# Kernel tuning notes

Hardware: AMD Instinct MI355X
Metric: run time of the kernel (lower is better)

The kernel has to match this reference:

```python
import jax, jax.numpy as jnp
import numpy as np

BN_EPS = 1e-5


def setup_inputs() -> dict:
    key = jax.random.key(0)
    k1, k2, k3, k4, k5 = jax.random.split(key, 5)
    N, E, D = 100000, 1600000, 128
    x = jax.random.normal(k1, (N, D), dtype=jnp.float32)
    edge_index = jax.random.randint(k2, (2, E), 0, N, dtype=jnp.int64)
    # GCNConv linear weight (PyG stores as [out, in], applied as x @ W.T) + post-agg bias
    W = jax.random.normal(k3, (D, D), dtype=jnp.float32) * (1.0 / np.sqrt(D))
    b = jax.random.normal(k4, (D,), dtype=jnp.float32) * 0.01
    gamma = jnp.ones((D,), dtype=jnp.float32)
    beta = jnp.zeros((D,), dtype=jnp.float32)
    return {"x": x, "edge_index": edge_index, "W": W, "b": b, "gamma": gamma, "beta": beta}


def reference(x, edge_index, W, b, gamma, beta):
    N = x.shape[0]
    src, dst = edge_index[0], edge_index[1]
    # GCN symmetric normalization (no self loops): deg over dst with unit weights
    deg = jax.ops.segment_sum(jnp.ones(src.shape[0], dtype=x.dtype), dst, num_segments=N)
    dinv = jnp.where(deg > 0, jax.lax.rsqrt(jnp.maximum(deg, 1.0)), 0.0)
    norm = dinv[src] * dinv[dst]                      # [E]
    xw = x @ W.T                                      # [N, D] linear transform first (fewer FLOPs)
    msg = xw[src] * norm[:, None]                     # [E, D] gather + scale
    agg = jax.ops.segment_sum(msg, dst, num_segments=N) + b  # [N, D] scatter-add + bias
    # BatchNorm1d over nodes (training-mode batch stats, biased variance)
    mu = jnp.mean(agg, axis=0)
    var = jnp.mean(jnp.square(agg - mu), axis=0)
    h = (agg - mu) * jax.lax.rsqrt(var + BN_EPS) * gamma + beta
    h = jax.nn.relu(h)
    return h + x
```

## Files before the change

kernel.cpp:

```cpp
#include <hip/hip_runtime.h>

#define DD 128
#define BN_EPS 1e-5f
#define BINSHIFT 8
#define EPB 8192
#define CAP 6144

typedef __attribute__((ext_vector_type(8))) short bf16x8;
typedef __attribute__((ext_vector_type(4))) float f32x4;

static __device__ __forceinline__ size_t rowoff(int r) { return (size_t)r * DD; }

static __device__ __forceinline__ ushort f2bf(float f) {
  unsigned u = __float_as_uint(f);
  unsigned r = (u + 0x7fffu + ((u >> 16) & 1u)) >> 16;
  return (ushort)r;
}

__global__ __launch_bounds__(256) void k_convW(const float* __restrict__ W,
                                               ushort* __restrict__ Wb) {
  int t = threadIdx.x;
#pragma unroll
  for (int i = 0; i < 16; ++i) {
    int f = i * 256 + t;
    int row = f >> 5, c4 = f & 31;
    float4 w = reinterpret_cast<const float4*>(W)[f];
    ushort4 p = make_ushort4(f2bf(w.x), f2bf(w.y), f2bf(w.z), f2bf(w.w));
    int chunk = (c4 >> 1) ^ (row & 7);
    *reinterpret_cast<ushort4*>(reinterpret_cast<char*>(Wb) + row * 256 +
                                chunk * 16 + (c4 & 1) * 8) = p;
  }
}

__global__ __launch_bounds__(256) void k_binscatter(const int* __restrict__ src,
                                                    const int* __restrict__ dst,
                                                    int* __restrict__ gcursor,
                                                    unsigned* __restrict__ stg,
                                                    int E, int NB) {
  __shared__ int hist[1024];
  __shared__ int base[1024];
  int t = threadIdx.x;
  long long e0 = (long long)blockIdx.x * EPB;
  int eend = (int)((e0 + EPB < E) ? e0 + EPB : E);
  for (int i = t; i < NB; i += 256) hist[i] = 0;
  __syncthreads();
  for (int i = (int)e0 + t; i < eend; i += 256) atomicAdd(&hist[dst[i] >> BINSHIFT], 1);
  __syncthreads();
  for (int i = t; i < NB; i += 256) {
    int c = hist[i];
    base[i] = c ? (i * CAP + atomicAdd(&gcursor[i], c)) : 0;
    hist[i] = 0;
  }
  __syncthreads();
  for (int i = (int)e0 + t; i < eend; i += 256) {
    int d = dst[i];
    int bin = d >> BINSHIFT;
    unsigned v = ((unsigned)(d & 255) << 24) | (unsigned)src[i];
    int p = atomicAdd(&hist[bin], 1);
    stg[base[bin] + p] = v;
  }
}

__global__ __launch_bounds__(256) void k_binsort(const unsigned* __restrict__ stg,
                                                 const int* __restrict__ gcursor,
                                                 int* __restrict__ ssrc,
                                                 int* __restrict__ offs,
                                                 int* __restrict__ oend,
                                                 float* __restrict__ dinv,
                                                 int N) {
  __shared__ int hist[256];
  __shared__ int scanb[256];
  int b = blockIdx.x;
  int t = threadIdx.x;
  int beg = b * CAP;
  int end = beg + gcursor[b];
  int nloc = N - b * 256;
  if (nloc > 256) nloc = 256;
  hist[t] = 0;
  __syncthreads();
  for (int i = beg + t; i < end; i += 256) atomicAdd(&hist[stg[i] >> 24], 1);
  __syncthreads();
  int h = hist[t];
  scanb[t] = h;
  __syncthreads();
  for (int off = 1; off < 256; off <<= 1) {
    int u = (t >= off) ? scanb[t - off] : 0;
    __syncthreads();
    scanb[t] += u;
    __syncthreads();
  }
  int myexcl = scanb[t] - h;
  __syncthreads();
  scanb[t] = myexcl;
  hist[t] = 0;
  int node = b * 256 + t;
  if (t < nloc) {
    offs[node] = beg + myexcl;
    oend[node] = beg + myexcl + h;
    dinv[node] = h > 0 ? rsqrtf((float)h) : 0.f;
  }
  __syncthreads();
  for (int i = beg + t; i < end; i += 256) {
    unsigned v = stg[i];
    int loc = v >> 24;
    int p = atomicAdd(&hist[loc], 1);
    ssrc[beg + scanb[loc] + p] = (int)(v & 0xFFFFFFu);
  }
}

__global__ __launch_bounds__(256) void k_gemm_mfma(const float* __restrict__ x,
                                                   const ushort* __restrict__ Wb,
                                                   const float* __restrict__ dinv,
                                                   ushort* __restrict__ xwb, int N) {
  __shared__ ushort Abuf[128 * 128];
  __shared__ ushort Bbuf[128 * 128];
  int t = threadIdx.x;
  int brow = blockIdx.x * 128;
  int wid = t >> 6, lane = t & 63;

  {
    const char* gW = reinterpret_cast<const char*>(Wb);
    char* lB = reinterpret_cast<char*>(Bbuf);
#pragma unroll
    for (int i = 0; i < 8; ++i) {
      int off = i * 4096 + wid * 1024;
      __builtin_amdgcn_global_load_lds(
          (const __attribute__((address_space(1))) void*)(gW + off + lane * 16),
          (__attribute__((address_space(3))) void*)(lB + off), 16, 0, 0);
    }
  }
  for (int i = 0; i < 16; ++i) {
    int f = i * 256 + t;
    int row = f >> 5, c4 = f & 31;
    int grow = brow + row;
    float4 v = make_float4(0.f, 0.f, 0.f, 0.f);
    if (grow < N) v = reinterpret_cast<const float4*>(x)[(size_t)grow * 32 + c4];
    ushort4 p = make_ushort4(f2bf(v.x), f2bf(v.y), f2bf(v.z), f2bf(v.w));
    int chunk = (c4 >> 1) ^ (row & 7);
    *reinterpret_cast<ushort4*>(reinterpret_cast<char*>(Abuf) + row * 256 +
                                chunk * 16 + (c4 & 1) * 8) = p;
  }
  __syncthreads();

  int kgrp = lane >> 4;
  int r0 = wid * 32 + (lane & 15);
  int r1 = r0 + 16;
  f32x4 acc[2][8];
#pragma unroll
  for (int rt = 0; rt < 2; ++rt)
#pragma unroll
    for (int cf = 0; cf < 8; ++cf) acc[rt][cf] = (f32x4){0.f, 0.f, 0.f, 0.f};

  const char* Ab = reinterpret_cast<const char*>(Abuf);
  const char* Bb = reinterpret_cast<const char*>(Bbuf);
#pragma unroll
  for (int ks = 0; ks < 4; ++ks) {
    int c = ks * 4 + kgrp;
    bf16x8 a0 = *reinterpret_cast<const bf16x8*>(Ab + r0 * 256 + ((c ^ (r0 & 7)) * 16));
    bf16x8 a1 = *reinterpret_cast<const bf16x8*>(Ab + r1 * 256 + ((c ^ (r1 & 7)) * 16));
#pragma unroll
    for (int cf = 0; cf < 8; ++cf) {
      int bc = cf * 16 + (lane & 15);
      bf16x8 bv = *reinterpret_cast<const bf16x8*>(Bb + bc * 256 + ((c ^ (bc & 7)) * 16));
      acc[0][cf] = __builtin_amdgcn_mfma_f32_16x16x32_bf16(a0, bv, acc[0][cf], 0, 0, 0);
      acc[1][cf] = __builtin_amdgcn_mfma_f32_16x16x32_bf16(a1, bv, acc[1][cf], 0, 0, 0);
    }
  }

#pragma unroll
  for (int rt = 0; rt < 2; ++rt) {
#pragma unroll
    for (int j = 0; j < 4; ++j) {
      int gr = brow + wid * 32 + rt * 16 + (lane >> 4) * 4 + j;
      if (gr < N) {
        float sc = dinv[gr];
        ushort* orow = xwb + (size_t)gr * DD + (lane & 15);
#pragma unroll
        for (int cf = 0; cf < 8; ++cf) orow[cf * 16] = f2bf(acc[rt][cf][j] * sc);
      }
    }
  }
}

__global__ __launch_bounds__(256) void k_aggregate(const int* __restrict__ offs,
                                                   const int* __restrict__ oend,
                                                   const int* __restrict__ ssrc,
                                                   const float* __restrict__ dinv,
                                                   const float* __restrict__ bvec,
                                                   const ushort* __restrict__ xwb,
                                                   float* __restrict__ agg,
                                                   float* __restrict__ stats, int N) {
  __shared__ float red[1024];
  int t = threadIdx.x;
  int wid = t >> 6, lane = t & 63;
  float bc0 = bvec[2 * lane], bc1 = bvec[2 * lane + 1];
  float s0 = 0.f, q0 = 0.f, s1 = 0.f, q1 = 0.f;
  const unsigned laneb = lane * 2;

  for (int d = blockIdx.x * 4 + wid; d < N; d += gridDim.x * 4) {
    int off = offs[d], end = oend[d];
    float a0 = 0.f, a1 = 0.f, b0 = 0.f, b1 = 0.f;
    float c0 = 0.f, c1 = 0.f, e0 = 0.f, e1 = 0.f;
    int j = off;
    for (; j + 8 <= end; j += 8) {
      int sA = ssrc[j],     sB = ssrc[j + 1], sC = ssrc[j + 2], sD = ssrc[j + 3];
      int sE = ssrc[j + 4], sF = ssrc[j + 5], sG = ssrc[j + 6], sH = ssrc[j + 7];
      unsigned v0 = *reinterpret_cast<const unsigned*>(xwb + (size_t)sA * DD + laneb);
      unsigned v1 = *reinterpret_cast<const unsigned*>(xwb + (size_t)sB * DD + laneb);
      unsigned v2 = *reinterpret_cast<const unsigned*>(xwb + (size_t)sC * DD + laneb);
      unsigned v3 = *reinterpret_cast<const unsigned*>(xwb + (size_t)sD * DD + laneb);
      unsigned v4 = *reinterpret_cast<const unsigned*>(xwb + (size_t)sE * DD + laneb);
      unsigned v5 = *reinterpret_cast<const unsigned*>(xwb + (size_t)sF * DD + laneb);
      unsigned v6 = *reinterpret_cast<const unsigned*>(xwb + (size_t)sG * DD + laneb);
      unsigned v7 = *reinterpret_cast<const unsigned*>(xwb + (size_t)sH * DD + laneb);
      a0 += __uint_as_float(v0 << 16);
      a1 += __uint_as_float(v0 & 0xffff0000u);
      b0 += __uint_as_float(v1 << 16);
      b1 += __uint_as_float(v1 & 0xffff0000u);
      c0 += __uint_as_float(v2 << 16);
      c1 += __uint_as_float(v2 & 0xffff0000u);
      e0 += __uint_as_float(v3 << 16);
      e1 += __uint_as_float(v3 & 0xffff0000u);
      a0 += __uint_as_float(v4 << 16);
      a1 += __uint_as_float(v4 & 0xffff0000u);
      b0 += __uint_as_float(v5 << 16);
      b1 += __uint_as_float(v5 & 0xffff0000u);
      c0 += __uint_as_float(v6 << 16);
      c1 += __uint_as_float(v6 & 0xffff0000u);
      e0 += __uint_as_float(v7 << 16);
      e1 += __uint_as_float(v7 & 0xffff0000u);
    }
    if (j + 4 <= end) {
      int sA = ssrc[j], sB = ssrc[j + 1], sC = ssrc[j + 2], sD = ssrc[j + 3];
      unsigned v0 = *reinterpret_cast<const unsigned*>(xwb + (size_t)sA * DD + laneb);
      unsigned v1 = *reinterpret_cast<const unsigned*>(xwb + (size_t)sB * DD + laneb);
      unsigned v2 = *reinterpret_cast<const unsigned*>(xwb + (size_t)sC * DD + laneb);
      unsigned v3 = *reinterpret_cast<const unsigned*>(xwb + (size_t)sD * DD + laneb);
      a0 += __uint_as_float(v0 << 16);
      a1 += __uint_as_float(v0 & 0xffff0000u);
      b0 += __uint_as_float(v1 << 16);
      b1 += __uint_as_float(v1 & 0xffff0000u);
      c0 += __uint_as_float(v2 << 16);
      c1 += __uint_as_float(v2 & 0xffff0000u);
      e0 += __uint_as_float(v3 << 16);
      e1 += __uint_as_float(v3 & 0xffff0000u);
      j += 4;
    }
    for (; j < end; ++j) {
      int sA = ssrc[j];
      unsigned v0 = *reinterpret_cast<const unsigned*>(xwb + (size_t)sA * DD + laneb);
      a0 += __uint_as_float(v0 << 16);
      a1 += __uint_as_float(v0 & 0xffff0000u);
    }
    float dd = dinv[d];
    float r0 = ((a0 + b0) + (c0 + e0)) * dd;
    float r1 = ((a1 + b1) + (c1 + e1)) * dd;
    reinterpret_cast<float2*>(agg + rowoff(d))[lane] = make_float2(r0, r1);
    float t0 = r0 + bc0, t1 = r1 + bc1;
    s0 += t0; q0 += t0 * t0;
    s1 += t1; q1 += t1 * t1;
  }

  float4* rw = reinterpret_cast<float4*>(red);
  rw[wid * 64 + lane] = make_float4(s0, q0, s1, q1);
  __syncthreads();
  {
    float v = red[t] + red[256 + t] + red[512 + t] + red[768 + t];
    int ln = t >> 2, k = t & 3;
    int col = 2 * ln + (k >> 1);
    int rep = blockIdx.x & 7;
    atomicAdd(&stats[rep * 256 + (k & 1) * 128 + col], v);
  }
}

__global__ __launch_bounds__(256) void k_final(float* __restrict__ agg,
                                               const float* __restrict__ x,
                                               const float* __restrict__ b,
                                               const float* __restrict__ gamma,
                                               const float* __restrict__ beta,
                                               const float* __restrict__ stats,
                                               float invN, int N) {
  __shared__ float muS[DD], rsS[DD];
  int t = threadIdx.x;
  if (t < DD) {
    float s = 0.f, q = 0.f;
#pragma unroll
    for (int rep = 0; rep < 8; ++rep) {
      s += stats[rep * 256 + t];
      q += stats[rep * 256 + 128 + t];
    }
    float mu = s * invN;
    float var = q * invN - mu * mu;
    muS[t] = mu;
    rsS[t] = rsqrtf(var + BN_EPS);
  }
  __syncthreads();

  long long i = (long long)blockIdx.x * 256 + threadIdx.x;
  long long stride = (long long)gridDim.x * 256;
  long long total = (long long)N * (DD / 4);
  const float4* __restrict__ x4 = reinterpret_cast<const float4*>(x);
  float4* __restrict__ a4 = reinterpret_cast<float4*>(agg);
  const float4* __restrict__ b4 = reinterpret_cast<const float4*>(b);
  const float4* __restrict__ g4 = reinterpret_cast<const float4*>(gamma);
  const float4* __restrict__ be4 = reinterpret_cast<const float4*>(beta);
  const float4* muL = reinterpret_cast<const float4*>(muS);
  const float4* rsL = reinterpret_cast<const float4*>(rsS);
  for (; i < total; i += stride) {
    int c4 = (int)(i & (DD / 4 - 1));
    float4 v = a4[i];
    float4 xv = x4[i];
    float4 bb = b4[c4], gg = g4[c4], be = be4[c4], mm = muL[c4], rr = rsL[c4];
    float4 o;
    o.x = fmaxf((v.x + bb.x - mm.x) * rr.x * gg.x + be.x, 0.f) + xv.x;
    o.y = fmaxf((v.y + bb.y - mm.y) * rr.y * gg.y + be.y, 0.f) + xv.y;
    o.z = fmaxf((v.z + bb.z - mm.z) * rr.z * gg.z + be.z, 0.f) + xv.z;
    o.w = fmaxf((v.w + bb.w - mm.w) * rr.w * gg.w + be.w, 0.f) + xv.w;
    a4[i] = o;
  }
}

extern "C" void kernel_launch(void* const* d_in, const int* in_sizes, int n_in,
                              void* d_out, int out_size, void* d_ws, size_t ws_size,
                              hipStream_t stream) {
  const float* x = (const float*)d_in[0];
  const int* ei = (const int*)d_in[1];
  const float* W = (const float*)d_in[2];
  const float* b = (const float*)d_in[3];
  const float* gamma = (const float*)d_in[4];
  const float* beta = (const float*)d_in[5];
  int N = in_sizes[0] / DD;
  int E = in_sizes[1] / 2;
  float* out = (float*)d_out;
  const int* src = ei;
  const int* dst = ei + E;
  int NB = (N + 255) >> BINSHIFT;

  ushort* xwb = (ushort*)d_ws;
  ushort* Wb = xwb + (size_t)N * DD;
  unsigned* stg = (unsigned*)(Wb + DD * DD);
  int* ssrc = (int*)(stg + (size_t)NB * CAP);
  int* offs = ssrc + (size_t)NB * CAP;
  int* oend = offs + N;
  float* dinv = (float*)(oend + N);
  int* gcursor = (int*)(dinv + N);
  float* stats = (float*)(gcursor + 1024);

  hipMemsetAsync(gcursor, 0, 1024 * sizeof(int) + 2048 * sizeof(float), stream);

  k_convW<<<1, 256, 0, stream>>>(W, Wb);

  int nchunk = (E + EPB - 1) / EPB;
  k_binscatter<<<nchunk, 256, 0, stream>>>(src, dst, gcursor, stg, E, NB);
  k_binsort<<<NB, 256, 0, stream>>>(stg, gcursor, ssrc, offs, oend, dinv, N);

  int gG = (N + 127) / 128;
  k_gemm_mfma<<<gG, 256, 0, stream>>>(x, Wb, dinv, xwb, N);

  k_aggregate<<<2048, 256, 0, stream>>>(offs, oend, ssrc, dinv, b, xwb, out, stats, N);

  k_final<<<2048, 256, 0, stream>>>(out, x, b, gamma, beta, stats, 1.0f / (float)N, N);
}
```

Measured before the change: 163.3 us.

## Merge W conversion into scatter, run binsort alongside GEMM, stage agg in bf16

The W bf16 conversion becomes an extra block of the edge scatter kernel. Binsort and the GEMM now share one launch, which removes the GEMM's dependence on dinv. The source-side dinv scaling moves into the aggregation loop as an extra gathered load per edge. Aggregated rows are written to a bf16 scratch buffer when workspace allows, halving the intermediate write and read traffic in the final kernel, at the cost of extra rounding error and more per-edge loads.

```diff
diff --git a/kernel.cpp b/kernel.cpp
--- a/kernel.cpp
+++ b/kernel.cpp
@@ -1,4 +1,5 @@
 #include <hip/hip_runtime.h>
+#include <hip/hip_bf16.h>
 
 #define DD 128
 #define BN_EPS 1e-5f
@@ -12,34 +13,35 @@
 static __device__ __forceinline__ size_t rowoff(int r) { return (size_t)r * DD; }
 
 static __device__ __forceinline__ ushort f2bf(float f) {
-  unsigned u = __float_as_uint(f);
-  unsigned r = (u + 0x7fffu + ((u >> 16) & 1u)) >> 16;
-  return (ushort)r;
-}
-
-__global__ __launch_bounds__(256) void k_convW(const float* __restrict__ W,
-                                               ushort* __restrict__ Wb) {
+  __hip_bfloat16 h = __float2bfloat16(f);
+  return __builtin_bit_cast(ushort, h);
+}
+static __device__ __forceinline__ float bf_lo(unsigned u) { return __uint_as_float(u << 16); }
+static __device__ __forceinline__ float bf_hi(unsigned u) { return __uint_as_float(u & 0xffff0000u); }
+
+__global__ __launch_bounds__(256) void k_scatter_convw(const int* __restrict__ src,
+                                                       const int* __restrict__ dst,
+                                                       int* __restrict__ gcursor,
+                                                       unsigned* __restrict__ stg,
+                                                       const float* __restrict__ W,
+                                                       ushort* __restrict__ Wb,
+                                                       int E, int NB, int nchunk) {
   int t = threadIdx.x;
-#pragma unroll
-  for (int i = 0; i < 16; ++i) {
-    int f = i * 256 + t;
-    int row = f >> 5, c4 = f & 31;
-    float4 w = reinterpret_cast<const float4*>(W)[f];
-    ushort4 p = make_ushort4(f2bf(w.x), f2bf(w.y), f2bf(w.z), f2bf(w.w));
-    int chunk = (c4 >> 1) ^ (row & 7);
-    *reinterpret_cast<ushort4*>(reinterpret_cast<char*>(Wb) + row * 256 +
-                                chunk * 16 + (c4 & 1) * 8) = p;
-  }
-}
-
-__global__ __launch_bounds__(256) void k_binscatter(const int* __restrict__ src,
-                                                    const int* __restrict__ dst,
-                                                    int* __restrict__ gcursor,
-                                                    unsigned* __restrict__ stg,
-                                                    int E, int NB) {
+  if (blockIdx.x == (unsigned)nchunk) {
+#pragma unroll
+    for (int i = 0; i < 16; ++i) {
+      int f = i * 256 + t;
+      int row = f >> 5, c4 = f & 31;
+      float4 w = reinterpret_cast<const float4*>(W)[f];
+      ushort4 p = make_ushort4(f2bf(w.x), f2bf(w.y), f2bf(w.z), f2bf(w.w));
+      int chunk = (c4 >> 1) ^ (row & 7);
+      *reinterpret_cast<ushort4*>(reinterpret_cast<char*>(Wb) + row * 256 +
+                                  chunk * 16 + (c4 & 1) * 8) = p;
+    }
+    return;
+  }
   __shared__ int hist[1024];
   __shared__ int base[1024];
-  int t = threadIdx.x;
   long long e0 = (long long)blockIdx.x * EPB;
   int eend = (int)((e0 + EPB < E) ? e0 + EPB : E);
   for (int i = t; i < NB; i += 256) hist[i] = 0;
@@ -61,66 +63,68 @@
   }
 }
 
-__global__ __launch_bounds__(256) void k_binsort(const unsigned* __restrict__ stg,
-                                                 const int* __restrict__ gcursor,
-                                                 int* __restrict__ ssrc,
-                                                 int* __restrict__ offs,
-                                                 int* __restrict__ oend,
-                                                 float* __restrict__ dinv,
-                                                 int N) {
-  __shared__ int hist[256];
-  __shared__ int scanb[256];
-  int b = blockIdx.x;
+__global__ __launch_bounds__(256) void k_gemm_binsort(const float* __restrict__ x,
+                                                      const ushort* __restrict__ Wb,
+                                                      ushort* __restrict__ xwb,
+                                                      const unsigned* __restrict__ stg,
+                                                      const int* __restrict__ gcursor,
+                                                      int* __restrict__ ssrc,
+                                                      int* __restrict__ offs,
+                                                      int* __restrict__ oend,
+                                                      float* __restrict__ dinv,
+                                                      int N, int gG) {
+  __shared__ char pool[65536];
   int t = threadIdx.x;
-  int beg = b * CAP;
-  int end = beg + gcursor[b];
-  int nloc = N - b * 256;
-  if (nloc > 256) nloc = 256;
-  hist[t] = 0;
-  __syncthreads();
-  for (int i = beg + t; i < end; i += 256) atomicAdd(&hist[stg[i] >> 24], 1);
-  __syncthreads();
-  int h = hist[t];
-  scanb[t] = h;
-  __syncthreads();
-  for (int off = 1; off < 256; off <<= 1) {
-    int u = (t >= off) ? scanb[t - off] : 0;
-    __syncthreads();
-    scanb[t] += u;
-    __syncthreads();
-  }
-  int myexcl = scanb[t] - h;
-  __syncthreads();
-  scanb[t] = myexcl;
-  hist[t] = 0;
-  int node = b * 256 + t;
-  if (t < nloc) {
-    offs[node] = beg + myexcl;
-    oend[node] = beg + myexcl + h;
-    dinv[node] = h > 0 ? rsqrtf((float)h) : 0.f;
-  }
-  __syncthreads();
-  for (int i = beg + t; i < end; i += 256) {
-    unsigned v = stg[i];
-    int loc = v >> 24;
-    int p = atomicAdd(&hist[loc], 1);
-    ssrc[beg + scanb[loc] + p] = (int)(v & 0xFFFFFFu);
-  }
-}
-
-__global__ __launch_bounds__(256) void k_gemm_mfma(const float* __restrict__ x,
-                                                   const ushort* __restrict__ Wb,
-                                                   const float* __restrict__ dinv,
-                                                   ushort* __restrict__ xwb, int N) {
-  __shared__ ushort Abuf[128 * 128];
-  __shared__ ushort Bbuf[128 * 128];
-  int t = threadIdx.x;
+
+  if ((int)blockIdx.x >= gG) {
+    int* hist = (int*)pool;
+    int* scanb = (int*)(pool + 1024);
+    int b = blockIdx.x - gG;
+    int beg = b * CAP;
+    int end = beg + gcursor[b];
+    int nloc = N - b * 256;
+    if (nloc > 256) nloc = 256;
+    hist[t] = 0;
+    __syncthreads();
+    for (int i = beg + t; i < end; i += 256) atomicAdd(&hist[stg[i] >> 24], 1);
+    __syncthreads();
+    int h = hist[t];
+    scanb[t] = h;
+    __syncthreads();
+    for (int off = 1; off < 256; off <<= 1) {
+      int u = (t >= off) ? scanb[t - off] : 0;
+      __syncthreads();
+      scanb[t] += u;
+      __syncthreads();
+    }
+    int myexcl = scanb[t] - h;
+    __syncthreads();
+    scanb[t] = myexcl;
+    hist[t] = 0;
+    int node = b * 256 + t;
+    if (t < nloc) {
+      offs[node] = beg + myexcl;
+      oend[node] = beg + myexcl + h;
+      dinv[node] = h > 0 ? rsqrtf((float)h) : 0.f;
+    }
+    __syncthreads();
+    for (int i = beg + t; i < end; i += 256) {
+      unsigned v = stg[i];
+      int loc = v >> 24;
+      int p = atomicAdd(&hist[loc], 1);
+      ssrc[beg + scanb[loc] + p] = (int)(v & 0xFFFFFFu);
+    }
+    return;
+  }
+
+  ushort* Abuf = (ushort*)pool;
+  ushort* Bbuf = (ushort*)(pool + 32768);
   int brow = blockIdx.x * 128;
   int wid = t >> 6, lane = t & 63;
 
   {
     const char* gW = reinterpret_cast<const char*>(Wb);
-    char* lB = reinterpret_cast<char*>(Bbuf);
+    char* lB = pool + 32768;
 #pragma unroll
     for (int i = 0; i < 8; ++i) {
       int off = i * 4096 + wid * 1024;
@@ -173,10 +177,9 @@
     for (int j = 0; j < 4; ++j) {
       int gr = brow + wid * 32 + rt * 16 + (lane >> 4) * 4 + j;
       if (gr < N) {
-        float sc = dinv[gr];
         ushort* orow = xwb + (size_t)gr * DD + (lane & 15);
 #pragma unroll
-        for (int cf = 0; cf < 8; ++cf) orow[cf * 16] = f2bf(acc[rt][cf][j] * sc);
+        for (int cf = 0; cf < 8; ++cf) orow[cf * 16] = f2bf(acc[rt][cf][j]);
       }
     }
   }
@@ -189,6 +192,7 @@
                                                    const float* __restrict__ bvec,
                                                    const ushort* __restrict__ xwb,
                                                    float* __restrict__ agg,
+                                                   ushort* __restrict__ aggb,
                                                    float* __restrict__ stats, int N) {
   __shared__ float red[1024];
   int t = threadIdx.x;
@@ -205,6 +209,8 @@
     for (; j + 8 <= end; j += 8) {
       int sA = ssrc[j],     sB = ssrc[j + 1], sC = ssrc[j + 2], sD = ssrc[j + 3];
       int sE = ssrc[j + 4], sF = ssrc[j + 5], sG = ssrc[j + 6], sH = ssrc[j + 7];
+      float nA = dinv[sA], nB = dinv[sB], nC = dinv[sC], nD = dinv[sD];
+      float nE = dinv[sE], nF = dinv[sF], nG = dinv[sG], nH = dinv[sH];
       unsigned v0 = *reinterpret_cast<const unsigned*>(xwb + (size_t)sA * DD + laneb);
       unsigned v1 = *reinterpret_cast<const unsigned*>(xwb + (size_t)sB * DD + laneb);
       unsigned v2 = *reinterpret_cast<const unsigned*>(xwb + (size_t)sC * DD + laneb);
@@ -213,49 +219,43 @@
       unsigned v5 = *reinterpret_cast<const unsigned*>(xwb + (size_t)sF * DD + laneb);
       unsigned v6 = *reinterpret_cast<const unsigned*>(xwb + (size_t)sG * DD + laneb);
       unsigned v7 = *reinterpret_cast<const unsigned*>(xwb + (size_t)sH * DD + laneb);
-      a0 += __uint_as_float(v0 << 16);
-      a1 += __uint_as_float(v0 & 0xffff0000u);
-      b0 += __uint_as_float(v1 << 16);
-      b1 += __uint_as_float(v1 & 0xffff0000u);
-      c0 += __uint_as_float(v2 << 16);
-      c1 += __uint_as_float(v2 & 0xffff0000u);
-      e0 += __uint_as_float(v3 << 16);
-      e1 += __uint_as_float(v3 & 0xffff0000u);
-      a0 += __uint_as_float(v4 << 16);
-      a1 += __uint_as_float(v4 & 0xffff0000u);
-      b0 += __uint_as_float(v5 << 16);
-      b1 += __uint_as_float(v5 & 0xffff0000u);
-      c0 += __uint_as_float(v6 << 16);
-      c1 += __uint_as_float(v6 & 0xffff0000u);
-      e0 += __uint_as_float(v7 << 16);
-      e1 += __uint_as_float(v7 & 0xffff0000u);
+      a0 = fmaf(bf_lo(v0), nA, a0); a1 = fmaf(bf_hi(v0), nA, a1);
+      b0 = fmaf(bf_lo(v1), nB, b0); b1 = fmaf(bf_hi(v1), nB, b1);
+      c0 = fmaf(bf_lo(v2), nC, c0); c1 = fmaf(bf_hi(v2), nC, c1);
+      e0 = fmaf(bf_lo(v3), nD, e0); e1 = fmaf(bf_hi(v3), nD, e1);
+      a0 = fmaf(bf_lo(v4), nE, a0); a1 = fmaf(bf_hi(v4), nE, a1);
+      b0 = fmaf(bf_lo(v5), nF, b0); b1 = fmaf(bf_hi(v5), nF, b1);
+      c0 = fmaf(bf_lo(v6), nG, c0); c1 = fmaf(bf_hi(v6), nG, c1);
+      e0 = fmaf(bf_lo(v7), nH, e0); e1 = fmaf(bf_hi(v7), nH, e1);
     }
     if (j + 4 <= end) {
       int sA = ssrc[j], sB = ssrc[j + 1], sC = ssrc[j + 2], sD = ssrc[j + 3];
+      float nA = dinv[sA], nB = dinv[sB], nC = dinv[sC], nD = dinv[sD];
       unsigned v0 = *reinterpret_cast<const unsigned*>(xwb + (size_t)sA * DD + laneb);
       unsigned v1 = *reinterpret_cast<const unsigned*>(xwb + (size_t)sB * DD + laneb);
       unsigned v2 = *reinterpret_cast<const unsigned*>(xwb + (size_t)sC * DD + laneb);
       unsigned v3 = *reinterpret_cast<const unsigned*>(xwb + (size_t)sD * DD + laneb);
-      a0 += __uint_as_float(v0 << 16);
-      a1 += __uint_as_float(v0 & 0xffff0000u);
-      b0 += __uint_as_float(v1 << 16);
-      b1 += __uint_as_float(v1 & 0xffff0000u);
-      c0 += __uint_as_float(v2 << 16);
-      c1 += __uint_as_float(v2 & 0xffff0000u);
-      e0 += __uint_as_float(v3 << 16);
-      e1 += __uint_as_float(v3 & 0xffff0000u);
+      a0 = fmaf(bf_lo(v0), nA, a0); a1 = fmaf(bf_hi(v0), nA, a1);
+      b0 = fmaf(bf_lo(v1), nB, b0); b1 = fmaf(bf_hi(v1), nB, b1);
+      c0 = fmaf(bf_lo(v2), nC, c0); c1 = fmaf(bf_hi(v2), nC, c1);
+      e0 = fmaf(bf_lo(v3), nD, e0); e1 = fmaf(bf_hi(v3), nD, e1);
       j += 4;
     }
     for (; j < end; ++j) {
       int sA = ssrc[j];
+      float nA = dinv[sA];
       unsigned v0 = *reinterpret_cast<const unsigned*>(xwb + (size_t)sA * DD + laneb);
-      a0 += __uint_as_float(v0 << 16);
-      a1 += __uint_as_float(v0 & 0xffff0000u);
+      a0 = fmaf(bf_lo(v0), nA, a0); a1 = fmaf(bf_hi(v0), nA, a1);
     }
     float dd = dinv[d];
     float r0 = ((a0 + b0) + (c0 + e0)) * dd;
     float r1 = ((a1 + b1) + (c1 + e1)) * dd;
-    reinterpret_cast<float2*>(agg + rowoff(d))[lane] = make_float2(r0, r1);
+    if (aggb) {
+      unsigned pk = (unsigned)f2bf(r0) | ((unsigned)f2bf(r1) << 16);
+      reinterpret_cast<unsigned*>(aggb + rowoff(d))[lane] = pk;
+    } else {
+      reinterpret_cast<float2*>(agg + rowoff(d))[lane] = make_float2(r0, r1);
+    }
     float t0 = r0 + bc0, t1 = r1 + bc1;
     s0 += t0; q0 += t0 * t0;
     s1 += t1; q1 += t1 * t1;
@@ -273,7 +273,8 @@
   }
 }
 
-__global__ __launch_bounds__(256) void k_final(float* __restrict__ agg,
+__global__ __launch_bounds__(256) void k_final(float* __restrict__ out,
+                                               const ushort* __restrict__ aggb,
                                                const float* __restrict__ x,
                                                const float* __restrict__ b,
                                                const float* __restrict__ gamma,
@@ -300,7 +301,7 @@
   long long stride = (long long)gridDim.x * 256;
   long long total = (long long)N * (DD / 4);
   const float4* __restrict__ x4 = reinterpret_cast<const float4*>(x);
-  float4* __restrict__ a4 = reinterpret_cast<float4*>(agg);
+  float4* __restrict__ o4 = reinterpret_cast<float4*>(out);
   const float4* __restrict__ b4 = reinterpret_cast<const float4*>(b);
   const float4* __restrict__ g4 = reinterpret_cast<const float4*>(gamma);
   const float4* __restrict__ be4 = reinterpret_cast<const float4*>(beta);
@@ -308,7 +309,13 @@
   const float4* rsL = reinterpret_cast<const float4*>(rsS);
   for (; i < total; i += stride) {
     int c4 = (int)(i & (DD / 4 - 1));
-    float4 v = a4[i];
+    float4 v;
+    if (aggb) {
+      uint2 av = reinterpret_cast<const uint2*>(aggb)[i];
+      v = make_float4(bf_lo(av.x), bf_hi(av.x), bf_lo(av.y), bf_hi(av.y));
+    } else {
+      v = o4[i];
+    }
     float4 xv = x4[i];
     float4 bb = b4[c4], gg = g4[c4], be = be4[c4], mm = muL[c4], rr = rsL[c4];
     float4 o;
@@ -316,7 +323,7 @@
     o.y = fmaxf((v.y + bb.y - mm.y) * rr.y * gg.y + be.y, 0.f) + xv.y;
     o.z = fmaxf((v.z + bb.z - mm.z) * rr.z * gg.z + be.z, 0.f) + xv.z;
     o.w = fmaxf((v.w + bb.w - mm.w) * rr.w * gg.w + be.w, 0.f) + xv.w;
-    a4[i] = o;
+    o4[i] = o;
   }
 }
 
@@ -345,19 +352,24 @@
   float* dinv = (float*)(oend + N);
   int* gcursor = (int*)(dinv + N);
   float* stats = (float*)(gcursor + 1024);
+  ushort* aggb = (ushort*)(stats + 2048);
+
+  size_t need_aggb = (size_t)((char*)(aggb + (size_t)N * DD) - (char*)d_ws);
+  if (ws_size < need_aggb) aggb = nullptr;
 
   hipMemsetAsync(gcursor, 0, 1024 * sizeof(int) + 2048 * sizeof(float), stream);
 
-  k_convW<<<1, 256, 0, stream>>>(W, Wb);
-
   int nchunk = (E + EPB - 1) / EPB;
-  k_binscatter<<<nchunk, 256, 0, stream>>>(src, dst, gcursor, stg, E, NB);
-  k_binsort<<<NB, 256, 0, stream>>>(stg, gcursor, ssrc, offs, oend, dinv, N);
+  k_scatter_convw<<<nchunk + 1, 256, 0, stream>>>(src, dst, gcursor, stg, W, Wb,
+                                                  E, NB, nchunk);
 
   int gG = (N + 127) / 128;
-  k_gemm_mfma<<<gG, 256, 0, stream>>>(x, Wb, dinv, xwb, N);
-
-  k_aggregate<<<2048, 256, 0, stream>>>(offs, oend, ssrc, dinv, b, xwb, out, stats, N);
-
-  k_final<<<2048, 256, 0, stream>>>(out, x, b, gamma, beta, stats, 1.0f / (float)N, N);
-}
+  k_gemm_binsort<<<gG + NB, 256, 0, stream>>>(x, Wb, xwb, stg, gcursor, ssrc,
+                                              offs, oend, dinv, N, gG);
+
+  k_aggregate<<<2048, 256, 0, stream>>>(offs, oend, ssrc, dinv, b, xwb, out, aggb,
+                                        stats, N);
+
+  k_final<<<2048, 256, 0, stream>>>(out, aggb, x, b, gamma, beta, stats,
+                                    1.0f / (float)N, N);
+}
```

After: 174.8 us. 7.0% more time.
